# Performance work log

Hardware: AMD Instinct MI355X
Metric: run time of the kernel (lower is better)

The kernel has to match this reference:

```python
import jax, jax.numpy as jnp
import numpy as np


def _schedule(epoch):
    # Mirrors SPLoss._adjust_N_ratio_q_t (epoch is a static Python int)
    if epoch <= 25:
        return 0.7, 2
    elif epoch <= 75:
        return 0.8, 0
    elif epoch <= 95:
        return 0.9, 0
    else:
        return 1.0, 0


def setup_inputs() -> dict:
    key = jax.random.key(0)
    k1, k2 = jax.random.split(key)
    B, C = 32768, 1000
    output = jax.random.normal(k1, (B, C), dtype=jnp.float32)
    target = jax.random.randint(k2, (B,), 0, C, dtype=jnp.int64)
    return {"output": output, "target": target, "epoch": 10}


def reference(output, target, epoch):
    N_ratio, q_t = _schedule(epoch)
    B = output.shape[0]
    # fused cross-entropy: log-softmax + per-sample gather
    logp = jax.nn.log_softmax(output, axis=-1)            # [B, C]
    ce_loss = -jnp.take_along_axis(logp, target[:, None], axis=1)[:, 0]  # [B]
    # sort-based quantile threshold
    sorted_ce = jnp.sort(ce_loss)                          # ascending
    lambda_t = sorted_ce[int(B * N_ratio)]
    # power reweight v_t = (1 - ce/lambda)^(1/(q_t-1)), zero past threshold, cap at 10
    exponent = 1.0 / (q_t - 1)
    v_t = (1.0 - ce_loss / lambda_t) ** exponent
    v_t = jnp.where(ce_loss >= lambda_t, 0.0, v_t)
    v_t = jnp.where(v_t >= 10.0, 10.0, v_t)
    return (ce_loss * v_t).mean()
```

## Files before the change

kernel.cpp:

```cpp
#include <hip/hip_runtime.h>
#include <math.h>


__device__ __forceinline__ unsigned f2u(float f) {
    unsigned u = __float_as_uint(f);
    return (u & 0x80000000u) ? ~u : (u | 0x80000000u);
}
__device__ __forceinline__ float u2f(unsigned u) {
    unsigned b = (u & 0x80000000u) ? (u & 0x7FFFFFFFu) : ~u;
    return __uint_as_float(b);
}

#define CE_WPB 4

__global__ __launch_bounds__(256) void ce_kernel(
        const float* __restrict__ x, const int* __restrict__ tgt,
        unsigned* __restrict__ ceu, unsigned* __restrict__ ghist, int B, int C)
{
    if (blockIdx.x == 0) {
        if (threadIdx.x < 256) ghist[threadIdx.x] = 0u;
        if (threadIdx.x == 0)  ghist[256] = 0u;
    }

    const int lane = threadIdx.x & 63;
    const int wave = threadIdx.x >> 6;
    const int row  = blockIdx.x * CE_WPB + wave;
    if (row >= B) return;

    const float* rp = x + (size_t)row * C;
    const int t = tgt[row];
    const float tv = rp[t];

    const int C4 = C >> 2;
    const float4* p4 = (const float4*)rp;
    const float NEG = -INFINITY;
    float4 v0 = make_float4(NEG, NEG, NEG, NEG), v1 = v0, v2 = v0, v3 = v0;
    if (lane       < C4) v0 = p4[lane];
    if (lane +  64 < C4) v1 = p4[lane + 64];
    if (lane + 128 < C4) v2 = p4[lane + 128];
    if (lane + 192 < C4) v3 = p4[lane + 192];

    float m = fmaxf(fmaxf(fmaxf(v0.x, v0.y), fmaxf(v0.z, v0.w)),
                    fmaxf(fmaxf(v1.x, v1.y), fmaxf(v1.z, v1.w)));
    m = fmaxf(m, fmaxf(fmaxf(v2.x, v2.y), fmaxf(v2.z, v2.w)));
    m = fmaxf(m, fmaxf(fmaxf(v3.x, v3.y), fmaxf(v3.z, v3.w)));
    for (int off = 32; off > 0; off >>= 1)
        m = fmaxf(m, __shfl_xor(m, off, 64));

    float s = __expf(v0.x - m) + __expf(v0.y - m) + __expf(v0.z - m) + __expf(v0.w - m)
            + __expf(v1.x - m) + __expf(v1.y - m) + __expf(v1.z - m) + __expf(v1.w - m)
            + __expf(v2.x - m) + __expf(v2.y - m) + __expf(v2.z - m) + __expf(v2.w - m)
            + __expf(v3.x - m) + __expf(v3.y - m) + __expf(v3.z - m) + __expf(v3.w - m);
    for (int off = 32; off > 0; off >>= 1)
        s += __shfl_xor(s, off, 64);

    if (lane == 0)
        ceu[row] = f2u((m + __logf(s)) - tv);
}

#define K2_T 1024
#define K2_W (K2_T / 64)
#define K2_B 16

__global__ __launch_bounds__(K2_T) void hist_select_kernel(
        const unsigned* __restrict__ ceu, unsigned* __restrict__ ghist,
        const int* __restrict__ epoch_p, float* __restrict__ out, int B)
{
    __shared__ unsigned wh[K2_W][256];
    __shared__ unsigned sv[32768];
    __shared__ unsigned sh[256];
    __shared__ unsigned s_prefix, s_k, s_old;
    __shared__ float    s_wsum[K2_W];

    const int tid  = threadIdx.x;
    const int lane = tid & 63;
    const int wave = tid >> 6;
    unsigned* ticket = ghist + 256;

    #pragma unroll
    for (int j = 0; j < 4; ++j) ((unsigned*)wh)[tid * 4 + j] = 0u;
    __syncthreads();

    const int n2 = B >> 1;
    for (int i = blockIdx.x * K2_T + tid; i < n2; i += gridDim.x * K2_T) {
        uint2 u = ((const uint2*)ceu)[i];
        atomicAdd(&wh[wave][u.x >> 24], 1u);
        atomicAdd(&wh[wave][u.y >> 24], 1u);
    }
    __syncthreads();

    if (tid < 256) {
        unsigned s = 0;
        #pragma unroll
        for (int w = 0; w < K2_W; ++w) s += wh[w][tid];
        if (s) atomicAdd(&ghist[tid], s);
    }
    __syncthreads();

    if (tid == 0)
        s_old = __hip_atomic_fetch_add(ticket, 1u,
                                       __ATOMIC_ACQ_REL, __HIP_MEMORY_SCOPE_AGENT);
    __syncthreads();
    if (s_old != gridDim.x - 1) return;

    const int n4 = B >> 2;
    for (int i = tid; i < n4; i += K2_T) ((uint4*)sv)[i] = ((const uint4*)ceu)[i];

    const int e = epoch_p[0];
    double nr; int qt;
    if (e <= 25)      { nr = 0.7; qt = 2; }
    else if (e <= 75) { nr = 0.8; qt = 0; }
    else if (e <= 95) { nr = 0.9; qt = 0; }
    else              { nr = 1.0; qt = 0; }
    const bool inv = (qt != 2);

    if (wave == 0) {
        long long kk = (long long)((double)B * nr);
        if (kk > (long long)B - 1) kk = (long long)B - 1;
        unsigned c0 = __hip_atomic_load(&ghist[4 * lane],     __ATOMIC_RELAXED, __HIP_MEMORY_SCOPE_AGENT);
        unsigned c1 = __hip_atomic_load(&ghist[4 * lane + 1], __ATOMIC_RELAXED, __HIP_MEMORY_SCOPE_AGENT);
        unsigned c2 = __hip_atomic_load(&ghist[4 * lane + 2], __ATOMIC_RELAXED, __HIP_MEMORY_SCOPE_AGENT);
        unsigned c3 = __hip_atomic_load(&ghist[4 * lane + 3], __ATOMIC_RELAXED, __HIP_MEMORY_SCOPE_AGENT);
        unsigned cw = c0 + c1 + c2 + c3;
        unsigned incl = cw;
        for (int off = 1; off < 64; off <<= 1) {
            unsigned t = __shfl_up(incl, off, 64);
            if (lane >= off) incl += t;
        }
        unsigned excl = incl - cw;
        unsigned kr = (unsigned)kk;
        unsigned long long bm = __ballot(excl <= kr && kr < excl + cw);
        int L = (int)(__ffsll((long long)bm) - 1);
        if (lane == L) {
            unsigned rem = kr - excl;
            int b; unsigned cum;
            if      (rem < c0)           { b = 0; cum = 0; }
            else if (rem < c0 + c1)      { b = 1; cum = c0; }
            else if (rem < c0 + c1 + c2) { b = 2; cum = c0 + c1; }
            else                         { b = 3; cum = c0 + c1 + c2; }
            s_k = rem - cum;
            s_prefix = (unsigned)(4 * L + b) << 24;
        }
    }
    __syncthreads();

    for (int p = 1; p < 4; ++p) {
        if (tid < 256) sh[tid] = 0u;
        __syncthreads();
        const int shift = 24 - 8 * p;
        const unsigned hm   = 0xFFFFFFFFu << (shift + 8);
        const unsigned pref = s_prefix;
        for (int j = tid; j < B; j += K2_T) {
            unsigned u = sv[j];
            if ((u & hm) == (pref & hm))
                atomicAdd(&sh[(u >> shift) & 255u], 1u);
        }
        __syncthreads();
        if (wave == 0) {
            unsigned c0 = sh[4 * lane], c1 = sh[4 * lane + 1];
            unsigned c2 = sh[4 * lane + 2], c3 = sh[4 * lane + 3];
            unsigned cw = c0 + c1 + c2 + c3;
            unsigned incl = cw;
            for (int off = 1; off < 64; off <<= 1) {
                unsigned t = __shfl_up(incl, off, 64);
                if (lane >= off) incl += t;
            }
            unsigned excl = incl - cw;
            unsigned kr = s_k;
            unsigned long long bm = __ballot(excl <= kr && kr < excl + cw);
            int L = (int)(__ffsll((long long)bm) - 1);
            if (lane == L) {
                unsigned rem = kr - excl;
                int b; unsigned cum;
                if      (rem < c0)           { b = 0; cum = 0; }
                else if (rem < c0 + c1)      { b = 1; cum = c0; }
                else if (rem < c0 + c1 + c2) { b = 2; cum = c0 + c1; }
                else                         { b = 3; cum = c0 + c1 + c2; }
                s_k = rem - cum;
                s_prefix = pref | ((unsigned)(4 * lane + b) << shift);
            }
        }
        __syncthreads();
    }

    const float lam = u2f(s_prefix);
    float part = 0.0f;
    for (int j = tid; j < B; j += K2_T) {
        float c = u2f(sv[j]);
        float base = 1.0f - c / lam;
        float v = inv ? (1.0f / base) : base;
        if (c >= lam)       v = 0.0f;
        else if (v >= 10.f) v = 10.0f;
        part += c * v;
    }
    for (int off = 32; off > 0; off >>= 1) part += __shfl_xor(part, off, 64);
    if (lane == 0) s_wsum[wave] = part;
    __syncthreads();
    if (tid == 0) {
        float tot = 0.0f;
        for (int i = 0; i < K2_W; ++i) tot += s_wsum[i];
        out[0] = tot / (float)B;
    }
}

extern "C" void kernel_launch(void* const* d_in, const int* in_sizes, int n_in,
                              void* d_out, int out_size, void* d_ws, size_t ws_size,
                              hipStream_t stream)
{
    const float* x     = (const float*)d_in[0];
    const int*   tgt   = (const int*)d_in[1];
    const int*   epoch = (const int*)d_in[2];
    int B = in_sizes[1];
    int C = in_sizes[0] / B;

    unsigned* ceu   = (unsigned*)d_ws;
    unsigned* ghist = ceu + B;

    int ceBlocks = (B + CE_WPB - 1) / CE_WPB;
    ce_kernel<<<ceBlocks, 256, 0, stream>>>(x, tgt, ceu, ghist, B, C);
    hist_select_kernel<<<K2_B, K2_T, 0, stream>>>(ceu, ghist, epoch,
                                                  (float*)d_out, B);
}
```

Baseline: 211.5 us.

## Fuse cross-entropy and histogram select into one persistent kernel with sliced global histogram

Merges the per-row cross-entropy kernel and the histogram/radix-select kernel into one persistent kernel with 1024 blocks of 256 threads. Each block builds the top-byte histogram while it computes CE values, then adds it into one of 16 global histogram slices to spread atomic contention. The last block, found by an atomic ticket, runs the refinement passes and the weighted sum. The zeroing moves to a hipMemsetAsync, and the final phase now runs on one 256-thread block reading ceu from global memory instead of a 1024-thread block with the values staged in LDS. That tail may be slower, traded against saving a kernel launch and a separate pass over ceu.

```diff
diff --git a/kernel.cpp b/kernel.cpp
--- a/kernel.cpp
+++ b/kernel.cpp
@@ -11,100 +11,93 @@
     return __uint_as_float(b);
 }
 
-#define CE_WPB 4
-
-__global__ __launch_bounds__(256) void ce_kernel(
+#define CE_BLOCKS 1024
+#define CE_T      256
+#define CE_W      4
+#define NSLICE    16
+
+__global__ __launch_bounds__(CE_T) void sploss_fused(
         const float* __restrict__ x, const int* __restrict__ tgt,
-        unsigned* __restrict__ ceu, unsigned* __restrict__ ghist, int B, int C)
+        const int* __restrict__ epoch_p, float* __restrict__ out,
+        unsigned* __restrict__ ceu, unsigned* __restrict__ ghist,
+        int B, int C)
 {
-    if (blockIdx.x == 0) {
-        if (threadIdx.x < 256) ghist[threadIdx.x] = 0u;
-        if (threadIdx.x == 0)  ghist[256] = 0u;
-    }
-
-    const int lane = threadIdx.x & 63;
-    const int wave = threadIdx.x >> 6;
-    const int row  = blockIdx.x * CE_WPB + wave;
-    if (row >= B) return;
-
-    const float* rp = x + (size_t)row * C;
-    const int t = tgt[row];
-    const float tv = rp[t];
-
-    const int C4 = C >> 2;
-    const float4* p4 = (const float4*)rp;
-    const float NEG = -INFINITY;
-    float4 v0 = make_float4(NEG, NEG, NEG, NEG), v1 = v0, v2 = v0, v3 = v0;
-    if (lane       < C4) v0 = p4[lane];
-    if (lane +  64 < C4) v1 = p4[lane + 64];
-    if (lane + 128 < C4) v2 = p4[lane + 128];
-    if (lane + 192 < C4) v3 = p4[lane + 192];
-
-    float m = fmaxf(fmaxf(fmaxf(v0.x, v0.y), fmaxf(v0.z, v0.w)),
-                    fmaxf(fmaxf(v1.x, v1.y), fmaxf(v1.z, v1.w)));
-    m = fmaxf(m, fmaxf(fmaxf(v2.x, v2.y), fmaxf(v2.z, v2.w)));
-    m = fmaxf(m, fmaxf(fmaxf(v3.x, v3.y), fmaxf(v3.z, v3.w)));
-    for (int off = 32; off > 0; off >>= 1)
-        m = fmaxf(m, __shfl_xor(m, off, 64));
-
-    float s = __expf(v0.x - m) + __expf(v0.y - m) + __expf(v0.z - m) + __expf(v0.w - m)
-            + __expf(v1.x - m) + __expf(v1.y - m) + __expf(v1.z - m) + __expf(v1.w - m)
-            + __expf(v2.x - m) + __expf(v2.y - m) + __expf(v2.z - m) + __expf(v2.w - m)
-            + __expf(v3.x - m) + __expf(v3.y - m) + __expf(v3.z - m) + __expf(v3.w - m);
-    for (int off = 32; off > 0; off >>= 1)
-        s += __shfl_xor(s, off, 64);
-
-    if (lane == 0)
-        ceu[row] = f2u((m + __logf(s)) - tv);
-}
-
-#define K2_T 1024
-#define K2_W (K2_T / 64)
-#define K2_B 16
-
-__global__ __launch_bounds__(K2_T) void hist_select_kernel(
-        const unsigned* __restrict__ ceu, unsigned* __restrict__ ghist,
-        const int* __restrict__ epoch_p, float* __restrict__ out, int B)
-{
-    __shared__ unsigned wh[K2_W][256];
-    __shared__ unsigned sv[32768];
+    __shared__ unsigned wh[CE_W][256];
     __shared__ unsigned sh[256];
     __shared__ unsigned s_prefix, s_k, s_old;
-    __shared__ float    s_wsum[K2_W];
+    __shared__ float    s_wsum[CE_W];
 
     const int tid  = threadIdx.x;
     const int lane = tid & 63;
     const int wave = tid >> 6;
-    unsigned* ticket = ghist + 256;
+    unsigned* ticket = ghist + NSLICE * 256;
 
     #pragma unroll
     for (int j = 0; j < 4; ++j) ((unsigned*)wh)[tid * 4 + j] = 0u;
     __syncthreads();
 
-    const int n2 = B >> 1;
-    for (int i = blockIdx.x * K2_T + tid; i < n2; i += gridDim.x * K2_T) {
-        uint2 u = ((const uint2*)ceu)[i];
-        atomicAdd(&wh[wave][u.x >> 24], 1u);
-        atomicAdd(&wh[wave][u.y >> 24], 1u);
-    }
+    const int wstride = CE_BLOCKS * CE_W;
+    const int C4 = C >> 2;
+    const float NEG = -INFINITY;
+
+    for (int row = blockIdx.x * CE_W + wave; row < B; row += wstride) {
+        const float* rp = x + (size_t)row * C;
+        const int t = tgt[row];
+        const float tv = rp[t];
+
+        const float4* p4 = (const float4*)rp;
+        float4 v0 = make_float4(NEG, NEG, NEG, NEG), v1 = v0, v2 = v0, v3 = v0;
+        if (lane       < C4) v0 = p4[lane];
+        if (lane +  64 < C4) v1 = p4[lane + 64];
+        if (lane + 128 < C4) v2 = p4[lane + 128];
+        if (lane + 192 < C4) v3 = p4[lane + 192];
+
+        float m = fmaxf(fmaxf(fmaxf(v0.x, v0.y), fmaxf(v0.z, v0.w)),
+                        fmaxf(fmaxf(v1.x, v1.y), fmaxf(v1.z, v1.w)));
+        m = fmaxf(m, fmaxf(fmaxf(v2.x, v2.y), fmaxf(v2.z, v2.w)));
+        m = fmaxf(m, fmaxf(fmaxf(v3.x, v3.y), fmaxf(v3.z, v3.w)));
+        for (int off = 32; off > 0; off >>= 1)
+            m = fmaxf(m, __shfl_xor(m, off, 64));
+
+        float s = __expf(v0.x - m) + __expf(v0.y - m) + __expf(v0.z - m) + __expf(v0.w - m)
+                + __expf(v1.x - m) + __expf(v1.y - m) + __expf(v1.z - m) + __expf(v1.w - m)
+                + __expf(v2.x - m) + __expf(v2.y - m) + __expf(v2.z - m) + __expf(v2.w - m)
+                + __expf(v3.x - m) + __expf(v3.y - m) + __expf(v3.z - m) + __expf(v3.w - m);
+        for (int off = 32; off > 0; off >>= 1)
+            s += __shfl_xor(s, off, 64);
+
+        if (lane == 0) {
+            unsigned cb = f2u((m + __logf(s)) - tv);
+            ceu[row] = cb;
+            atomicAdd(&wh[wave][cb >> 24], 1u);
+        }
+    }
+    __syncthreads();
+
+    if (tid < 256) {
+        unsigned s = wh[0][tid] + wh[1][tid] + wh[2][tid] + wh[3][tid];
+        if (s) atomicAdd(&ghist[(blockIdx.x & (NSLICE - 1)) * 256 + tid], s);
+    }
+    __syncthreads();
+
+    if (tid == 0)
+        s_old = __hip_atomic_fetch_add(ticket, 1u,
+                                       __ATOMIC_ACQ_REL, __HIP_MEMORY_SCOPE_AGENT);
+    __syncthreads();
+    if (s_old != (unsigned)(gridDim.x - 1)) return;
+
+    __threadfence();
     __syncthreads();
 
     if (tid < 256) {
         unsigned s = 0;
         #pragma unroll
-        for (int w = 0; w < K2_W; ++w) s += wh[w][tid];
-        if (s) atomicAdd(&ghist[tid], s);
-    }
-    __syncthreads();
-
-    if (tid == 0)
-        s_old = __hip_atomic_fetch_add(ticket, 1u,
-                                       __ATOMIC_ACQ_REL, __HIP_MEMORY_SCOPE_AGENT);
-    __syncthreads();
-    if (s_old != gridDim.x - 1) return;
-
-    const int n4 = B >> 2;
-    for (int i = tid; i < n4; i += K2_T) ((uint4*)sv)[i] = ((const uint4*)ceu)[i];
+        for (int i = 0; i < NSLICE; ++i)
+            s += __hip_atomic_load(&ghist[i * 256 + tid],
+                                   __ATOMIC_RELAXED, __HIP_MEMORY_SCOPE_AGENT);
+        sh[tid] = s;
+    }
+    __syncthreads();
 
     const int e = epoch_p[0];
     double nr; int qt;
@@ -117,10 +110,8 @@
     if (wave == 0) {
         long long kk = (long long)((double)B * nr);
         if (kk > (long long)B - 1) kk = (long long)B - 1;
-        unsigned c0 = __hip_atomic_load(&ghist[4 * lane],     __ATOMIC_RELAXED, __HIP_MEMORY_SCOPE_AGENT);
-        unsigned c1 = __hip_atomic_load(&ghist[4 * lane + 1], __ATOMIC_RELAXED, __HIP_MEMORY_SCOPE_AGENT);
-        unsigned c2 = __hip_atomic_load(&ghist[4 * lane + 2], __ATOMIC_RELAXED, __HIP_MEMORY_SCOPE_AGENT);
-        unsigned c3 = __hip_atomic_load(&ghist[4 * lane + 3], __ATOMIC_RELAXED, __HIP_MEMORY_SCOPE_AGENT);
+        unsigned c0 = sh[4 * lane],     c1 = sh[4 * lane + 1];
+        unsigned c2 = sh[4 * lane + 2], c3 = sh[4 * lane + 3];
         unsigned cw = c0 + c1 + c2 + c3;
         unsigned incl = cw;
         for (int off = 1; off < 64; off <<= 1) {
@@ -150,8 +141,8 @@
         const int shift = 24 - 8 * p;
         const unsigned hm   = 0xFFFFFFFFu << (shift + 8);
         const unsigned pref = s_prefix;
-        for (int j = tid; j < B; j += K2_T) {
-            unsigned u = sv[j];
+        for (int j = tid; j < B; j += CE_T) {
+            unsigned u = ceu[j];
             if ((u & hm) == (pref & hm))
                 atomicAdd(&sh[(u >> shift) & 255u], 1u);
         }
@@ -185,8 +176,8 @@
 
     const float lam = u2f(s_prefix);
     float part = 0.0f;
-    for (int j = tid; j < B; j += K2_T) {
-        float c = u2f(sv[j]);
+    for (int j = tid; j < B; j += CE_T) {
+        float c = u2f(ceu[j]);
         float base = 1.0f - c / lam;
         float v = inv ? (1.0f / base) : base;
         if (c >= lam)       v = 0.0f;
@@ -198,7 +189,7 @@
     __syncthreads();
     if (tid == 0) {
         float tot = 0.0f;
-        for (int i = 0; i < K2_W; ++i) tot += s_wsum[i];
+        for (int i = 0; i < CE_W; ++i) tot += s_wsum[i];
         out[0] = tot / (float)B;
     }
 }
@@ -216,8 +207,7 @@
     unsigned* ceu   = (unsigned*)d_ws;
     unsigned* ghist = ceu + B;
 
-    int ceBlocks = (B + CE_WPB - 1) / CE_WPB;
-    ce_kernel<<<ceBlocks, 256, 0, stream>>>(x, tgt, ceu, ghist, B, C);
-    hist_select_kernel<<<K2_B, K2_T, 0, stream>>>(ceu, ghist, epoch,
-                                                  (float*)d_out, B);
-}
+    (void)hipMemsetAsync(ghist, 0, (NSLICE * 256 + 1) * sizeof(unsigned), stream);
+    sploss_fused<<<CE_BLOCKS, CE_T, 0, stream>>>(x, tgt, epoch,
+                                                 (float*)d_out, ceu, ghist, B, C);
+}
```

Result: slower. 336.7 us (+59.2%).
